# Optimization experiments

Hardware: AMD Instinct MI355X
Metric: run time of the kernel (lower is better)

## Reference

```python
import jax, jax.numpy as jnp
import numpy as np

B, I, J, C, H = 1, 384, 384, 128, 4
CH = 128          # overall hidden
HD = CH // H      # 32 per head
INF = 1000000000.0
EPS = 1e-5


def setup_inputs() -> dict:
    key = jax.random.key(0)
    ks = jax.random.split(key, 10)
    s = 0.02
    return {
        "x": jax.random.normal(ks[0], (B, I, J, C), dtype=jnp.float32),
        "mask": jnp.ones((B, I, J), dtype=jnp.float32),
        "ln_w": jnp.ones((C,), dtype=jnp.float32),
        "ln_b": jnp.zeros((C,), dtype=jnp.float32),
        "wz": jax.random.normal(ks[1], (C, H), dtype=jnp.float32) * s,
        "bz": jnp.zeros((H,), dtype=jnp.float32),
        "wq": jax.random.normal(ks[2], (C, CH), dtype=jnp.float32) * s,
        "wk": jax.random.normal(ks[3], (C, CH), dtype=jnp.float32) * s,
        "wv": jax.random.normal(ks[4], (C, CH), dtype=jnp.float32) * s,
        "wg": jax.random.normal(ks[5], (C, CH), dtype=jnp.float32) * s,
        "bg": jnp.ones((CH,), dtype=jnp.float32),
        "wo": jax.random.normal(ks[6], (CH, C), dtype=jnp.float32) * s,
        "bo": jnp.zeros((C,), dtype=jnp.float32),
    }


def _layer_norm(x, w, b):
    mu = jnp.mean(x, axis=-1, keepdims=True)
    var = jnp.mean(jnp.square(x - mu), axis=-1, keepdims=True)
    return (x - mu) * jax.lax.rsqrt(var + EPS) * w + b


def reference(x, mask, ln_w, ln_b, wz, bz, wq, wk, wv, wg, bg, wo, bo):
    # starting=True: attention over last row axis J
    x = _layer_norm(x, ln_w, ln_b)                      # [B,I,J,C]
    mask_bias = (INF * (mask - 1.0))[:, :, None, None, :]   # [B,I,1,1,J]
    # triangle bias: linear_z then permute (2,0,1), unsqueeze(-4) -> [B,1,H,I,J]
    tri_bias = jnp.einsum("bijc,ch->bhij", x, wz) + bz[None, :, None, None]
    tri_bias = tri_bias[:, None]                        # [B,1,H,I,J]

    q = jnp.einsum("bijc,cd->bijd", x, wq).reshape(B, I, J, H, HD)
    k = jnp.einsum("bijc,cd->bijd", x, wk).reshape(B, I, J, H, HD)
    v = jnp.einsum("bijc,cd->bijd", x, wv).reshape(B, I, J, H, HD)
    q = q / jnp.sqrt(jnp.float32(HD))

    a = jnp.einsum("biqhd,bikhd->bihqk", q, k)          # [B,I,H,J,J]
    a = a + mask_bias + tri_bias
    a = jax.nn.softmax(a, axis=-1)
    o = jnp.einsum("bihqk,bikhd->biqhd", a, v)          # [B,I,J,H,HD]

    g = jax.nn.sigmoid(jnp.einsum("bijc,cd->bijd", x, wg) + bg)
    o = o.reshape(B, I, J, CH) * g
    return jnp.einsum("bijd,dc->bijc", o, wo) + bo      # [B,I,J,C]
```

## Files before the change

kernel.cpp:

```cpp
#include <hip/hip_runtime.h>
#include <math.h>

#define I_DIM 384
#define C_DIM 128
#define H_NUM 4
#define HD_DIM 32
#define M_DIM (I_DIM*I_DIM)
#define INF_F 1000000000.0f
#define EPS_F 1e-5f
#define QSCALE 0.17677669529663687f

typedef __attribute__((ext_vector_type(8))) short short8;
typedef __attribute__((ext_vector_type(4))) float f32x4;
union U4S8 { uint4 u; short8 s; };

__device__ __forceinline__ unsigned short f2bf(float f) {
    unsigned int u = __float_as_uint(f);
    u += 0x7fffu + ((u >> 16) & 1u);
    return (unsigned short)(u >> 16);
}
__device__ __forceinline__ float bf2f(unsigned short h) {
    return __uint_as_float((unsigned int)h << 16);
}
__device__ __forceinline__ unsigned int pk2(float a, float b) {
    return (unsigned int)f2bf(a) | ((unsigned int)f2bf(b) << 16);
}
__device__ __forceinline__ unsigned int cvtpk(float lo, float hi) {
    unsigned int r;
    asm("v_cvt_pk_bf16_f32 %0, %1, %2" : "=v"(r) : "v"(lo), "v"(hi));
    return r;
}

__device__ uint4 wfmt_dev[5*4096];

__device__ __forceinline__ void load_lds16(const uint4* gp, void* lp) {
    __builtin_amdgcn_global_load_lds(
        (const __attribute__((address_space(1))) unsigned int*)gp,
        (__attribute__((address_space(3))) unsigned int*)lp,
        16, 0, 0);
}

__global__ __launch_bounds__(256) void wprep_kernel(
    const float* __restrict__ wq, const float* __restrict__ wk,
    const float* __restrict__ wg, const float* __restrict__ wv,
    const float* __restrict__ wo)
{
    const int tid  = blockIdx.x*256 + threadIdx.x;
    const int l    = tid & 63, tile = tid >> 6;
    const int ks   = tile & 3, nt = (tile >> 2) & 7;
    const int s    = (tile >> 5) & 1, m = tile >> 6;
    const float* W = (m==0)?wq:(m==1)?wk:(m==2)?wg:(m==3)?wv:wo;
    const float scale = (m==0) ? QSCALE : 1.f;
    const int n  = nt*16 + (l & 15);
    const int kb = ks*32 + (l >> 4)*8;
    unsigned int hw[4];
    #pragma unroll
    for (int jp = 0; jp < 4; ++jp) {
        unsigned short hs[2];
        #pragma unroll
        for (int e = 0; e < 2; ++e) {
            float v = W[(size_t)(kb + jp*2 + e)*C_DIM + n] * scale;
            unsigned short h = f2bf(v);
            if (s) h = f2bf(v - bf2f(h));
            hs[e] = h;
        }
        hw[jp] = (unsigned int)hs[0] | ((unsigned int)hs[1] << 16);
    }
    wfmt_dev[(size_t)m*4096 + (size_t)((s*8 + nt)*4 + ks)*64 + l] =
        make_uint4(hw[0], hw[1], hw[2], hw[3]);
}

__global__ __launch_bounds__(256, 4) void ln_proj_kernel(
    const float* __restrict__ x,
    const float* __restrict__ lnw, const float* __restrict__ lnb,
    const float* __restrict__ wz,  const float* __restrict__ bz,
    const float* __restrict__ bg,
    float* __restrict__ qo, unsigned short* __restrict__ ko16,
    unsigned int* __restrict__ vto, float* __restrict__ go,
    float* __restrict__ zo)
{
    __shared__ __align__(16) unsigned int xs[4096];
    __shared__ __align__(16) uint4 wbuf4[1024];
    unsigned int* vts = xs;

    const int t    = threadIdx.x;
    const int row0 = blockIdx.x * 64;
    const int w = t >> 6, l = t & 63, n16 = l & 15, quad = l >> 4;

    #pragma unroll
    for (int it = 0; it < 4; ++it) {
        const int tl = w*4 + it;
        const int s = tl >> 3, ntl = (tl >> 2) & 1, ks = tl & 3;
        load_lds16(wfmt_dev + (size_t)((s*8 + ntl)*4 + ks)*64 + l,
                   (char*)wbuf4 + tl*1024);
    }

    float4 xv[8];
    const int r = t >> 2, qt = t & 3, c0 = qt * 32;
    const int sw = (r & 7) << 2;
    {
        const float* xrow = x + (size_t)(row0 + r)*C_DIM + c0;
        float s = 0.f, ss = 0.f;
        #pragma unroll
        for (int i2 = 0; i2 < 8; i2++) {
            xv[i2] = ((const float4*)xrow)[i2];
            s  += xv[i2].x + xv[i2].y + xv[i2].z + xv[i2].w;
            ss += xv[i2].x*xv[i2].x + xv[i2].y*xv[i2].y
                + xv[i2].z*xv[i2].z + xv[i2].w*xv[i2].w;
        }
        s  += __shfl_xor(s, 1);  s  += __shfl_xor(s, 2);
        ss += __shfl_xor(ss, 1); ss += __shfl_xor(ss, 2);
        const float mean = s * (1.f/128.f);
        const float var  = ss * (1.f/128.f) - mean*mean;
        const float rstd = rsqrtf(var + EPS_F);
        const float4* wz4 = (const float4*)wz;
        float4 zacc = make_float4(0.f,0.f,0.f,0.f);
        #pragma unroll
        for (int i2 = 0; i2 < 8; i2++) {
            float4 w4 = ((const float4*)(lnw + c0))[i2];
            float4 b4 = ((const float4*)(lnb + c0))[i2];
            float4 r4;
            r4.x = (xv[i2].x - mean)*rstd*w4.x + b4.x;
            r4.y = (xv[i2].y - mean)*rstd*w4.y + b4.y;
            r4.z = (xv[i2].z - mean)*rstd*w4.z + b4.z;
            r4.w = (xv[i2].w - mean)*rstd*w4.w + b4.w;
            const float4 za = wz4[c0 + i2*4 + 0];
            const float4 zb_ = wz4[c0 + i2*4 + 1];
            const float4 zc = wz4[c0 + i2*4 + 2];
            const float4 zd = wz4[c0 + i2*4 + 3];
            zacc.x += r4.x*za.x + r4.y*zb_.x + r4.z*zc.x + r4.w*zd.x;
            zacc.y += r4.x*za.y + r4.y*zb_.y + r4.z*zc.y + r4.w*zd.y;
            zacc.z += r4.x*za.z + r4.y*zb_.z + r4.z*zc.z + r4.w*zd.z;
            zacc.w += r4.x*za.w + r4.y*zb_.w + r4.z*zc.w + r4.w*zd.w;
            const int wi = r*64 + qt*16 + i2*2;
            xs[(wi  ) ^ sw] = pk2(r4.x, r4.y);
            xs[(wi+1) ^ sw] = pk2(r4.z, r4.w);
            xv[i2] = r4;
        }
        zacc.x += __shfl_xor(zacc.x, 1); zacc.x += __shfl_xor(zacc.x, 2);
        zacc.y += __shfl_xor(zacc.y, 1); zacc.y += __shfl_xor(zacc.y, 2);
        zacc.z += __shfl_xor(zacc.z, 1); zacc.z += __shfl_xor(zacc.z, 2);
        zacc.w += __shfl_xor(zacc.w, 1); zacc.w += __shfl_xor(zacc.w, 2);
        const float zv = (qt==0)?zacc.x:(qt==1)?zacc.y:(qt==2)?zacc.z:zacc.w;
        zo[(size_t)qt*M_DIM + row0 + r] = zv + bz[qt];
    }
    __syncthreads();

    U4S8 ah[4], al[4];
    const int arow = w*16 + n16;
    #pragma unroll
    for (int ks = 0; ks < 4; ++ks) {
        const int bofs = arow*256 + ((ks*64 + quad*16) ^ ((arow & 7) << 4));
        ah[ks].u = *(const uint4*)((const char*)xs + bofs);
    }
    __syncthreads();

    #pragma unroll
    for (int i2 = 0; i2 < 8; i2++) {
        const float4 r4 = xv[i2];
        const unsigned short h0 = f2bf(r4.x), h1 = f2bf(r4.y),
                             h2 = f2bf(r4.z), h3 = f2bf(r4.w);
        const int wi = r*64 + qt*16 + i2*2;
        xs[(wi  ) ^ sw] = (unsigned int)f2bf(r4.x - bf2f(h0))
                        | ((unsigned int)f2bf(r4.y - bf2f(h1)) << 16);
        xs[(wi+1) ^ sw] = (unsigned int)f2bf(r4.z - bf2f(h2))
                        | ((unsigned int)f2bf(r4.w - bf2f(h3)) << 16);
    }
    __syncthreads();
    #pragma unroll
    for (int ks = 0; ks < 4; ++ks) {
        const int bofs = arow*256 + ((ks*64 + quad*16) ^ ((arow & 7) << 4));
        al[ks].u = *(const uint4*)((const char*)xs + bofs);
    }

    const int i_blk = row0 / I_DIM;
    const int jp0   = (row0 % I_DIM) >> 1;
    const int rw0   = row0 + w*16 + quad*4;

    #pragma unroll
    for (int rd = 0; rd < 16; ++rd) {
        const int mi = rd >> 2, qq = rd & 3;

        f32x4 acc[2];
        #pragma unroll
        for (int ntl = 0; ntl < 2; ++ntl) {
            f32x4 a = {0.f, 0.f, 0.f, 0.f};
            #pragma unroll
            for (int ks = 0; ks < 4; ++ks) {
                U4S8 bh, bl;
                bh.u = wbuf4[(    ntl*4 + ks)*64 + l];
                bl.u = wbuf4[(8 + ntl*4 + ks)*64 + l];
                a = __builtin_amdgcn_mfma_f32_16x16x32_bf16(ah[ks].s, bh.s, a, 0,0,0);
                a = __builtin_amdgcn_mfma_f32_16x16x32_bf16(al[ks].s, bh.s, a, 0,0,0);
                a = __builtin_amdgcn_mfma_f32_16x16x32_bf16(ah[ks].s, bl.s, a, 0,0,0);
            }
            acc[ntl] = a;
        }

        if (mi == 0) {
            #pragma unroll
            for (int ntl = 0; ntl < 2; ++ntl)
                #pragma unroll
                for (int rr = 0; rr < 4; ++rr)
                    qo[(size_t)(rw0 + rr)*C_DIM + qq*32 + ntl*16 + n16] =
                        acc[ntl][rr];
        } else if (mi == 1) {
            #pragma unroll
            for (int ntl = 0; ntl < 2; ++ntl)
                #pragma unroll
                for (int rr = 0; rr < 4; ++rr)
                    ko16[(size_t)(rw0 + rr)*C_DIM + qq*32 + ntl*16 + n16] =
                        f2bf(acc[ntl][rr]);
        } else if (mi == 2) {
            #pragma unroll
            for (int ntl = 0; ntl < 2; ++ntl) {
                const float bgv = bg[qq*32 + ntl*16 + n16];
                #pragma unroll
                for (int rr = 0; rr < 4; ++rr)
                    go[(size_t)(rw0 + rr)*C_DIM + qq*32 + ntl*16 + n16] =
                        1.f/(1.f + __expf(-(acc[ntl][rr] + bgv)));
            }
        } else {
            #pragma unroll
            for (int ntl = 0; ntl < 2; ++ntl)
                #pragma unroll
                for (int pr = 0; pr < 2; ++pr)
                    vts[(ntl*16 + n16)*33 + w*8 + quad*2 + pr] =
                        pk2(acc[ntl][2*pr], acc[ntl][2*pr+1]);
            __syncthreads();
            for (int idx = t; idx < 32*32; idx += 256) {
                const int ch_l = idx >> 5, p = idx & 31;
                vto[((size_t)i_blk*C_DIM + qq*32 + ch_l)*192 + jp0 + p] =
                    vts[ch_l*33 + p];
            }
        }

        __syncthreads();
        if (rd < 15) {
            const int m2 = (rd+1) >> 2, q2 = (rd+1) & 3;
            #pragma unroll
            for (int it = 0; it < 4; ++it) {
                const int tl = w*4 + it;
                const int s = tl >> 3, ntl2 = (tl >> 2) & 1, ks = tl & 3;
                load_lds16(wfmt_dev + (size_t)m2*4096
                           + (size_t)((s*8 + (q2*2 + ntl2))*4 + ks)*64 + l,
                           (char*)wbuf4 + tl*1024);
            }
        }
        __syncthreads();
    }
}

__global__ __launch_bounds__(256, 3) void attn_mfma_kernel(
    const float* q, const unsigned short* __restrict__ k16,
    const unsigned int* __restrict__ vt32, const float* __restrict__ zb,
    const float* __restrict__ mask, float* o)
{
    __shared__ uint4 Ks4[384*4];
    __shared__ uint4 VTl[32*49];
    __shared__ __align__(16) float mbl[384];

    const int ii = blockIdx.x;
    const int h  = blockIdx.y;
    const int t  = threadIdx.x;
    const size_t rbase = (size_t)ii*I_DIM*C_DIM + h*HD_DIM;

    for (int idx = t; idx < 1536; idx += 256) {
        const int j = idx >> 2, c4 = idx & 3;
        Ks4[j*4 + (c4 ^ ((j >> 1) & 3))] =
            ((const uint4*)k16)[rbase/8 + (size_t)j*16 + c4];
    }
    for (int idx = t; idx < 1536; idx += 256) {
        const int d = idx / 48, m = idx - d*48;
        VTl[d*49 + m] = ((const uint4*)vt32)[((size_t)ii*C_DIM + h*HD_DIM + d)*48 + m];
    }
    for (int jj = t; jj < 384; jj += 256)
        mbl[jj] = INF_F * (mask[(size_t)ii*I_DIM + jj] - 1.f);
    __syncthreads();

    const int w = t >> 6, l = t & 63;
    const int n16 = l & 15, quad = l >> 4;
    const int slA = n16 + ((quad & 1) << 5);
    const int slB = slA + 16;
    const bool hi = (quad & 2) != 0;

    #pragma unroll 1
    for (int qt = 0; qt < 6; qt++) {
        const int qg = w*6 + qt;

        U4S8 a;
        {
            const float* qrow = q + rbase + (size_t)(qg*16 + n16)*C_DIM + quad*8;
            const float4 f0 = ((const float4*)qrow)[0];
            const float4 f1 = ((const float4*)qrow)[1];
            a.u = make_uint4(cvtpk(f0.x,f0.y), cvtpk(f0.z,f0.w),
                             cvtpk(f1.x,f1.y), cvtpk(f1.z,f1.w));
        }

        f32x4 oacc0 = {0.f,0.f,0.f,0.f}, oacc1 = {0.f,0.f,0.f,0.f};
        float lsum = 0.f;
        const float* zrow = zb + (size_t)h*M_DIM
                          + (size_t)(qg*16 + n16)*I_DIM + quad*4;

        #pragma unroll 1
        for (int c = 0; c < 4; c++) {
            float4 zc4[6];
            #pragma unroll
            for (int k6 = 0; k6 < 6; k6++)
                zc4[k6] = *(const float4*)&zrow[96*c + k6*16];
            float4 mb4[6];
            #pragma unroll
            for (int k6 = 0; k6 < 6; k6++)
                mb4[k6] = *(const float4*)&mbl[96*c + k6*16 + quad*4];

            f32x4 accS[6];
            #pragma unroll
            for (int k6 = 0; k6 < 6; k6++) {
                const int key = (6*c + k6)*16 + n16;
                U4S8 b;
                b.u = Ks4[key*4 + (quad ^ ((key >> 1) & 3))];
                accS[k6] = __builtin_amdgcn_mfma_f32_16x16x32_bf16(
                    b.s, a.s, (f32x4){0.f,0.f,0.f,0.f}, 0, 0, 0);
            }

            unsigned int pu[6][2];
            #pragma unroll
            for (int k6 = 0; k6 < 6; k6++) {
                const float e0 = __expf(accS[k6][0] + zc4[k6].x + mb4[k6].x);
                const float e1 = __expf(accS[k6][1] + zc4[k6].y + mb4[k6].y);
                const float e2 = __expf(accS[k6][2] + zc4[k6].z + mb4[k6].z);
                const float e3 = __expf(accS[k6][3] + zc4[k6].w + mb4[k6].w);
                lsum += (e0 + e1) + (e2 + e3);
                pu[k6][0] = cvtpk(e0, e1);
                pu[k6][1] = cvtpk(e2, e3);
            }

            #pragma unroll
            for (int km = 0; km < 3; km++) {
                const unsigned int x0 = __shfl((int)pu[2*km  ][0], slA);
                const unsigned int x1 = __shfl((int)pu[2*km+1][0], slA);
                const unsigned int y0 = __shfl((int)pu[2*km  ][1], slA);
                const unsigned int y1 = __shfl((int)pu[2*km+1][1], slA);
                const unsigned int z0 = __shfl((int)pu[2*km  ][0], slB);
                const unsigned int z1 = __shfl((int)pu[2*km+1][0], slB);
                const unsigned int w0 = __shfl((int)pu[2*km  ][1], slB);
                const unsigned int w1 = __shfl((int)pu[2*km+1][1], slB);
                U4S8 pa;
                pa.u = make_uint4(hi?x1:x0, hi?y1:y0, hi?z1:z0, hi?w1:w0);
                U4S8 vb0, vb1;
                vb0.u = VTl[(n16     )*49 + quad + 4*km + 12*c];
                vb1.u = VTl[(16 + n16)*49 + quad + 4*km + 12*c];
                oacc0 = __builtin_amdgcn_mfma_f32_16x16x32_bf16(vb0.s, pa.s, oacc0, 0,0,0);
                oacc1 = __builtin_amdgcn_mfma_f32_16x16x32_bf16(vb1.s, pa.s, oacc1, 0,0,0);
            }
        }

        float s_ = lsum;
        s_ += __shfl_xor(s_, 16);
        s_ += __shfl_xor(s_, 32);
        const float rcp = 1.f / s_;
        const size_t orow = rbase + (size_t)(qg*16 + n16)*C_DIM;
        float4 o0 = make_float4(oacc0[0]*rcp, oacc0[1]*rcp,
                                oacc0[2]*rcp, oacc0[3]*rcp);
        float4 o1 = make_float4(oacc1[0]*rcp, oacc1[1]*rcp,
                                oacc1[2]*rcp, oacc1[3]*rcp);
        *(float4*)&o[orow + quad*4]      = o0;
        *(float4*)&o[orow + 16 + quad*4] = o1;
    }
}

__global__ __launch_bounds__(256, 4) void out_proj_kernel(
    const float* __restrict__ o, const float* g,
    const float* __restrict__ bo, float* out)
{
    __shared__ __align__(16) unsigned int xs[4096];
    __shared__ __align__(16) uint4 wbuf4[1024];
    const int t    = threadIdx.x;
    const int row0 = blockIdx.x * 64;
    const int w = t >> 6, l = t & 63, n16 = l & 15, quad = l >> 4;

    #pragma unroll
    for (int it = 0; it < 4; ++it) {
        const int tl = w*4 + it;
        const int s = tl >> 3, ntl = (tl >> 2) & 1, ks = tl & 3;
        load_lds16(wfmt_dev + (size_t)4*4096 + (size_t)((s*8 + ntl)*4 + ks)*64 + l,
                   (char*)wbuf4 + tl*1024);
    }

    float4 pv[8];
    const int r = t >> 2, qt = t & 3, c0 = qt * 32;
    const int sw = (r & 7) << 2;
    {
        const float4* orow = (const float4*)(o + (size_t)(row0 + r)*C_DIM + c0);
        const float4* grow = (const float4*)(g + (size_t)(row0 + r)*C_DIM + c0);
        #pragma unroll
        for (int i2 = 0; i2 < 8; i2++) {
            const float4 a = orow[i2];
            const float4 b = grow[i2];
            float4 p;
            p.x = a.x*b.x; p.y = a.y*b.y; p.z = a.z*b.z; p.w = a.w*b.w;
            const int wi = r*64 + qt*16 + i2*2;
            xs[(wi  ) ^ sw] = pk2(p.x, p.y);
            xs[(wi+1) ^ sw] = pk2(p.z, p.w);
            pv[i2] = p;
        }
    }
    __syncthreads();

    U4S8 ah[4], al[4];
    const int arow = w*16 + n16;
    #pragma unroll
    for (int ks = 0; ks < 4; ++ks) {
        const int bofs = arow*256 + ((ks*64 + quad*16) ^ ((arow & 7) << 4));
        ah[ks].u = *(const uint4*)((const char*)xs + bofs);
    }
    __syncthreads();
    #pragma unroll
    for (int i2 = 0; i2 < 8; i2++) {
        const float4 p = pv[i2];
        const unsigned short h0 = f2bf(p.x), h1 = f2bf(p.y),
                             h2 = f2bf(p.z), h3 = f2bf(p.w);
        const int wi = r*64 + qt*16 + i2*2;
        xs[(wi  ) ^ sw] = (unsigned int)f2bf(p.x - bf2f(h0))
                        | ((unsigned int)f2bf(p.y - bf2f(h1)) << 16);
        xs[(wi+1) ^ sw] = (unsigned int)f2bf(p.z - bf2f(h2))
                        | ((unsigned int)f2bf(p.w - bf2f(h3)) << 16);
    }
    __syncthreads();
    #pragma unroll
    for (int ks = 0; ks < 4; ++ks) {
        const int bofs = arow*256 + ((ks*64 + quad*16) ^ ((arow & 7) << 4));
        al[ks].u = *(const uint4*)((const char*)xs + bofs);
    }

    const int rw0 = row0 + w*16 + quad*4;
    #pragma unroll
    for (int qq = 0; qq < 4; ++qq) {
        f32x4 acc[2];
        #pragma unroll
        for (int ntl = 0; ntl < 2; ++ntl) {
            f32x4 a = {0.f, 0.f, 0.f, 0.f};
            #pragma unroll
            for (int ks = 0; ks < 4; ++ks) {
                U4S8 bh, bl;
                bh.u = wbuf4[(    ntl*4 + ks)*64 + l];
                bl.u = wbuf4[(8 + ntl*4 + ks)*64 + l];
                a = __builtin_amdgcn_mfma_f32_16x16x32_bf16(ah[ks].s, bh.s, a, 0,0,0);
                a = __builtin_amdgcn_mfma_f32_16x16x32_bf16(al[ks].s, bh.s, a, 0,0,0);
                a = __builtin_amdgcn_mfma_f32_16x16x32_bf16(ah[ks].s, bl.s, a, 0,0,0);
            }
            acc[ntl] = a;
        }
        #pragma unroll
        for (int ntl = 0; ntl < 2; ++ntl) {
            const int n = qq*32 + ntl*16 + n16;
            const float bov = bo[n];
            #pragma unroll
            for (int rr = 0; rr < 4; ++rr)
                out[(size_t)(rw0 + rr)*C_DIM + n] = acc[ntl][rr] + bov;
        }
        __syncthreads();
        if (qq < 3) {
            const int q2 = qq + 1;
            #pragma unroll
            for (int it = 0; it < 4; ++it) {
                const int tl = w*4 + it;
                const int s = tl >> 3, ntl2 = (tl >> 2) & 1, ks = tl & 3;
                load_lds16(wfmt_dev + (size_t)4*4096
                           + (size_t)((s*8 + (q2*2 + ntl2))*4 + ks)*64 + l,
                           (char*)wbuf4 + tl*1024);
            }
        }
        __syncthreads();
    }
}

extern "C" void kernel_launch(void* const* d_in, const int* in_sizes, int n_in,
                              void* d_out, int out_size, void* d_ws, size_t ws_size,
                              hipStream_t stream)
{
    (void)in_sizes; (void)n_in; (void)out_size; (void)ws_size;
    const float* x    = (const float*)d_in[0];
    const float* mask = (const float*)d_in[1];
    const float* lnw  = (const float*)d_in[2];
    const float* lnb  = (const float*)d_in[3];
    const float* wz   = (const float*)d_in[4];
    const float* bz   = (const float*)d_in[5];
    const float* wq   = (const float*)d_in[6];
    const float* wk   = (const float*)d_in[7];
    const float* wv   = (const float*)d_in[8];
    const float* wg   = (const float*)d_in[9];
    const float* bg   = (const float*)d_in[10];
    const float* wo   = (const float*)d_in[11];
    const float* bo   = (const float*)d_in[12];

    float* ws = (float*)d_ws;
    float* qb   = ws;
    float* zbuf = qb + (size_t)M_DIM*C_DIM;
    unsigned short* kb16 = (unsigned short*)(zbuf + (size_t)H_NUM*M_DIM);
    unsigned int*   vt32 = (unsigned int*)(kb16 + (size_t)M_DIM*C_DIM);
    float* gbuf = (float*)d_out;

    wprep_kernel<<<80, 256, 0, stream>>>(wq, wk, wg, wv, wo);
    ln_proj_kernel<<<M_DIM/64, 256, 0, stream>>>(
        x, lnw, lnb, wz, bz, bg, qb, kb16, vt32, gbuf, zbuf);
    attn_mfma_kernel<<<dim3(I_DIM, H_NUM), 256, 0, stream>>>(
        qb, kb16, vt32, zbuf, mask, qb );
    out_proj_kernel<<<M_DIM/64, 256, 0, stream>>>(
        qb, gbuf, bo, (float*)d_out);
}
```

Baseline: 440.9 us.

## Double-buffer weight tiles, use exp2 softmax, read K from global, swizzle V LDS

The projection and output kernels now double-buffer the weight tiles in LDS. The next tile's async load is issued before the current MFMA work, and one barrier per iteration is dropped. This doubles weight LDS and lowers launch-bounds occupancy from 4 to 3. The attention kernel folds log2(e) into the Q scale, triangle bias and mask so it can use the native exp2. It reads K fragments straight from global instead of staging them in LDS, and stores V^T in a swizzled fragment layout to avoid bank conflicts, with occupancy raised to 4.

```diff
diff --git a/kernel.cpp b/kernel.cpp
--- a/kernel.cpp
+++ b/kernel.cpp
@@ -9,6 +9,7 @@
 #define INF_F 1000000000.0f
 #define EPS_F 1e-5f
 #define QSCALE 0.17677669529663687f
+#define LOG2E_F 1.4426950408889634f
 
 typedef __attribute__((ext_vector_type(8))) short short8;
 typedef __attribute__((ext_vector_type(4))) float f32x4;
@@ -50,7 +51,7 @@
     const int ks   = tile & 3, nt = (tile >> 2) & 7;
     const int s    = (tile >> 5) & 1, m = tile >> 6;
     const float* W = (m==0)?wq:(m==1)?wk:(m==2)?wg:(m==3)?wv:wo;
-    const float scale = (m==0) ? QSCALE : 1.f;
+    const float scale = (m==0) ? QSCALE*LOG2E_F : 1.f;
     const int n  = nt*16 + (l & 15);
     const int kb = ks*32 + (l >> 4)*8;
     unsigned int hw[4];
@@ -70,7 +71,7 @@
         make_uint4(hw[0], hw[1], hw[2], hw[3]);
 }
 
-__global__ __launch_bounds__(256, 4) void ln_proj_kernel(
+__global__ __launch_bounds__(256, 3) void ln_proj_kernel(
     const float* __restrict__ x,
     const float* __restrict__ lnw, const float* __restrict__ lnb,
     const float* __restrict__ wz,  const float* __restrict__ bz,
@@ -80,7 +81,7 @@
     float* __restrict__ zo)
 {
     __shared__ __align__(16) unsigned int xs[4096];
-    __shared__ __align__(16) uint4 wbuf4[1024];
+    __shared__ __align__(16) uint4 wbuf4[2048];
     unsigned int* vts = xs;
 
     const int t    = threadIdx.x;
@@ -142,7 +143,7 @@
         zacc.z += __shfl_xor(zacc.z, 1); zacc.z += __shfl_xor(zacc.z, 2);
         zacc.w += __shfl_xor(zacc.w, 1); zacc.w += __shfl_xor(zacc.w, 2);
         const float zv = (qt==0)?zacc.x:(qt==1)?zacc.y:(qt==2)?zacc.z:zacc.w;
-        zo[(size_t)qt*M_DIM + row0 + r] = zv + bz[qt];
+        zo[(size_t)qt*M_DIM + row0 + r] = (zv + bz[qt]) * LOG2E_F;
     }
     __syncthreads();
 
@@ -177,10 +178,23 @@
     const int jp0   = (row0 % I_DIM) >> 1;
     const int rw0   = row0 + w*16 + quad*4;
 
+    int p = 0;
     #pragma unroll
     for (int rd = 0; rd < 16; ++rd) {
         const int mi = rd >> 2, qq = rd & 3;
 
+        if (rd < 15) {
+            const int m2 = (rd+1) >> 2, q2 = (rd+1) & 3;
+            #pragma unroll
+            for (int it = 0; it < 4; ++it) {
+                const int tl = w*4 + it;
+                const int s = tl >> 3, ntl2 = (tl >> 2) & 1, ks = tl & 3;
+                load_lds16(wfmt_dev + (size_t)m2*4096
+                           + (size_t)((s*8 + (q2*2 + ntl2))*4 + ks)*64 + l,
+                           (char*)wbuf4 + (p^1)*16384 + tl*1024);
+            }
+        }
+
         f32x4 acc[2];
         #pragma unroll
         for (int ntl = 0; ntl < 2; ++ntl) {
@@ -188,8 +202,8 @@
             #pragma unroll
             for (int ks = 0; ks < 4; ++ks) {
                 U4S8 bh, bl;
-                bh.u = wbuf4[(    ntl*4 + ks)*64 + l];
-                bl.u = wbuf4[(8 + ntl*4 + ks)*64 + l];
+                bh.u = wbuf4[p*1024 + (    ntl*4 + ks)*64 + l];
+                bl.u = wbuf4[p*1024 + (8 + ntl*4 + ks)*64 + l];
                 a = __builtin_amdgcn_mfma_f32_16x16x32_bf16(ah[ks].s, bh.s, a, 0,0,0);
                 a = __builtin_amdgcn_mfma_f32_16x16x32_bf16(al[ks].s, bh.s, a, 0,0,0);
                 a = __builtin_amdgcn_mfma_f32_16x16x32_bf16(ah[ks].s, bl.s, a, 0,0,0);
@@ -229,35 +243,23 @@
                         pk2(acc[ntl][2*pr], acc[ntl][2*pr+1]);
             __syncthreads();
             for (int idx = t; idx < 32*32; idx += 256) {
-                const int ch_l = idx >> 5, p = idx & 31;
-                vto[((size_t)i_blk*C_DIM + qq*32 + ch_l)*192 + jp0 + p] =
-                    vts[ch_l*33 + p];
+                const int ch_l = idx >> 5, pp = idx & 31;
+                vto[((size_t)i_blk*C_DIM + qq*32 + ch_l)*192 + jp0 + pp] =
+                    vts[ch_l*33 + pp];
             }
         }
 
         __syncthreads();
-        if (rd < 15) {
-            const int m2 = (rd+1) >> 2, q2 = (rd+1) & 3;
-            #pragma unroll
-            for (int it = 0; it < 4; ++it) {
-                const int tl = w*4 + it;
-                const int s = tl >> 3, ntl2 = (tl >> 2) & 1, ks = tl & 3;
-                load_lds16(wfmt_dev + (size_t)m2*4096
-                           + (size_t)((s*8 + (q2*2 + ntl2))*4 + ks)*64 + l,
-                           (char*)wbuf4 + tl*1024);
-            }
-        }
-        __syncthreads();
-    }
-}
-
-__global__ __launch_bounds__(256, 3) void attn_mfma_kernel(
+        p ^= 1;
+    }
+}
+
+__global__ __launch_bounds__(256, 4) void attn_mfma_kernel(
     const float* q, const unsigned short* __restrict__ k16,
     const unsigned int* __restrict__ vt32, const float* __restrict__ zb,
     const float* __restrict__ mask, float* o)
 {
-    __shared__ uint4 Ks4[384*4];
-    __shared__ uint4 VTl[32*49];
+    __shared__ uint4 VTf[24*64];
     __shared__ __align__(16) float mbl[384];
 
     const int ii = blockIdx.x;
@@ -266,16 +268,18 @@
     const size_t rbase = (size_t)ii*I_DIM*C_DIM + h*HD_DIM;
 
     for (int idx = t; idx < 1536; idx += 256) {
-        const int j = idx >> 2, c4 = idx & 3;
-        Ks4[j*4 + (c4 ^ ((j >> 1) & 3))] =
-            ((const uint4*)k16)[rbase/8 + (size_t)j*16 + c4];
-    }
-    for (int idx = t; idx < 1536; idx += 256) {
         const int d = idx / 48, m = idx - d*48;
-        VTl[d*49 + m] = ((const uint4*)vt32)[((size_t)ii*C_DIM + h*HD_DIM + d)*48 + m];
+        const int c = m / 12, rr = m - c*12;
+        const int km = rr >> 2, qd = rr & 3;
+        const int hh = d >> 4, nn = d & 15;
+        const int f  = (c*3 + km)*2 + hh;
+        const int l0 = qd*16 + nn;
+        const int lp = l0 ^ ((l0 >> 3) & 7) ^ ((3*c + km) & 7);
+        VTf[f*64 + lp] =
+            ((const uint4*)vt32)[((size_t)ii*C_DIM + h*HD_DIM + d)*48 + m];
     }
     for (int jj = t; jj < 384; jj += 256)
-        mbl[jj] = INF_F * (mask[(size_t)ii*I_DIM + jj] - 1.f);
+        mbl[jj] = (INF_F*LOG2E_F) * (mask[(size_t)ii*I_DIM + jj] - 1.f);
     __syncthreads();
 
     const int w = t >> 6, l = t & 63;
@@ -283,6 +287,8 @@
     const int slA = n16 + ((quad & 1) << 5);
     const int slB = slA + 16;
     const bool hi = (quad & 2) != 0;
+    const int lswz = l ^ ((l >> 3) & 7);
+    const unsigned short* kf = k16 + rbase + (size_t)n16*C_DIM + quad*8;
 
     #pragma unroll 1
     for (int qt = 0; qt < 6; qt++) {
@@ -304,6 +310,10 @@
 
         #pragma unroll 1
         for (int c = 0; c < 4; c++) {
+            U4S8 kb[6];
+            #pragma unroll
+            for (int k6 = 0; k6 < 6; k6++)
+                kb[k6].u = *(const uint4*)(kf + (size_t)((6*c + k6)*16)*C_DIM);
             float4 zc4[6];
             #pragma unroll
             for (int k6 = 0; k6 < 6; k6++)
@@ -315,21 +325,17 @@
 
             f32x4 accS[6];
             #pragma unroll
+            for (int k6 = 0; k6 < 6; k6++)
+                accS[k6] = __builtin_amdgcn_mfma_f32_16x16x32_bf16(
+                    kb[k6].s, a.s, (f32x4){0.f,0.f,0.f,0.f}, 0, 0, 0);
+
+            unsigned int pu[6][2];
+            #pragma unroll
             for (int k6 = 0; k6 < 6; k6++) {
-                const int key = (6*c + k6)*16 + n16;
-                U4S8 b;
-                b.u = Ks4[key*4 + (quad ^ ((key >> 1) & 3))];
-                accS[k6] = __builtin_amdgcn_mfma_f32_16x16x32_bf16(
-                    b.s, a.s, (f32x4){0.f,0.f,0.f,0.f}, 0, 0, 0);
-            }
-
-            unsigned int pu[6][2];
-            #pragma unroll
-            for (int k6 = 0; k6 < 6; k6++) {
-                const float e0 = __expf(accS[k6][0] + zc4[k6].x + mb4[k6].x);
-                const float e1 = __expf(accS[k6][1] + zc4[k6].y + mb4[k6].y);
-                const float e2 = __expf(accS[k6][2] + zc4[k6].z + mb4[k6].z);
-                const float e3 = __expf(accS[k6][3] + zc4[k6].w + mb4[k6].w);
+                const float e0 = __builtin_amdgcn_exp2f(accS[k6][0] + zc4[k6].x + mb4[k6].x);
+                const float e1 = __builtin_amdgcn_exp2f(accS[k6][1] + zc4[k6].y + mb4[k6].y);
+                const float e2 = __builtin_amdgcn_exp2f(accS[k6][2] + zc4[k6].z + mb4[k6].z);
+                const float e3 = __builtin_amdgcn_exp2f(accS[k6][3] + zc4[k6].w + mb4[k6].w);
                 lsum += (e0 + e1) + (e2 + e3);
                 pu[k6][0] = cvtpk(e0, e1);
                 pu[k6][1] = cvtpk(e2, e3);
@@ -347,9 +353,10 @@
                 const unsigned int w1 = __shfl((int)pu[2*km+1][1], slB);
                 U4S8 pa;
                 pa.u = make_uint4(hi?x1:x0, hi?y1:y0, hi?z1:z0, hi?w1:w0);
+                const int mix = (3*c + km) & 7;
                 U4S8 vb0, vb1;
-                vb0.u = VTl[(n16     )*49 + quad + 4*km + 12*c];
-                vb1.u = VTl[(16 + n16)*49 + quad + 4*km + 12*c];
+                vb0.u = VTf[((c*3 + km)*2    )*64 + (lswz ^ mix)];
+                vb1.u = VTf[((c*3 + km)*2 + 1)*64 + (lswz ^ mix)];
                 oacc0 = __builtin_amdgcn_mfma_f32_16x16x32_bf16(vb0.s, pa.s, oacc0, 0,0,0);
                 oacc1 = __builtin_amdgcn_mfma_f32_16x16x32_bf16(vb1.s, pa.s, oacc1, 0,0,0);
             }
@@ -369,12 +376,12 @@
     }
 }
 
-__global__ __launch_bounds__(256, 4) void out_proj_kernel(
+__global__ __launch_bounds__(256, 3) void out_proj_kernel(
     const float* __restrict__ o, const float* g,
     const float* __restrict__ bo, float* out)
 {
     __shared__ __align__(16) unsigned int xs[4096];
-    __shared__ __align__(16) uint4 wbuf4[1024];
+    __shared__ __align__(16) uint4 wbuf4[2048];
     const int t    = threadIdx.x;
     const int row0 = blockIdx.x * 64;
     const int w = t >> 6, l = t & 63, n16 = l & 15, quad = l >> 4;
@@ -434,32 +441,9 @@
     }
 
     const int rw0 = row0 + w*16 + quad*4;
+    int p = 0;
     #pragma unroll
     for (int qq = 0; qq < 4; ++qq) {
-        f32x4 acc[2];
-        #pragma unroll
-        for (int ntl = 0; ntl < 2; ++ntl) {
-            f32x4 a = {0.f, 0.f, 0.f, 0.f};
-            #pragma unroll
-            for (int ks = 0; ks < 4; ++ks) {
-                U4S8 bh, bl;
-                bh.u = wbuf4[(    ntl*4 + ks)*64 + l];
-                bl.u = wbuf4[(8 + ntl*4 + ks)*64 + l];
-                a = __builtin_amdgcn_mfma_f32_16x16x32_bf16(ah[ks].s, bh.s, a, 0,0,0);
-                a = __builtin_amdgcn_mfma_f32_16x16x32_bf16(al[ks].s, bh.s, a, 0,0,0);
-                a = __builtin_amdgcn_mfma_f32_16x16x32_bf16(ah[ks].s, bl.s, a, 0,0,0);
-            }
-            acc[ntl] = a;
-        }
-        #pragma unroll
-        for (int ntl = 0; ntl < 2; ++ntl) {
-            const int n = qq*32 + ntl*16 + n16;
-            const float bov = bo[n];
-            #pragma unroll
-            for (int rr = 0; rr < 4; ++rr)
-                out[(size_t)(rw0 + rr)*C_DIM + n] = acc[ntl][rr] + bov;
-        }
-        __syncthreads();
         if (qq < 3) {
             const int q2 = qq + 1;
             #pragma unroll
@@ -468,10 +452,34 @@
                 const int s = tl >> 3, ntl2 = (tl >> 2) & 1, ks = tl & 3;
                 load_lds16(wfmt_dev + (size_t)4*4096
                            + (size_t)((s*8 + (q2*2 + ntl2))*4 + ks)*64 + l,
-                           (char*)wbuf4 + tl*1024);
-            }
+                           (char*)wbuf4 + (p^1)*16384 + tl*1024);
+            }
+        }
+        f32x4 acc[2];
+        #pragma unroll
+        for (int ntl = 0; ntl < 2; ++ntl) {
+            f32x4 a = {0.f, 0.f, 0.f, 0.f};
+            #pragma unroll
+            for (int ks = 0; ks < 4; ++ks) {
+                U4S8 bh, bl;
+                bh.u = wbuf4[p*1024 + (    ntl*4 + ks)*64 + l];
+                bl.u = wbuf4[p*1024 + (8 + ntl*4 + ks)*64 + l];
+                a = __builtin_amdgcn_mfma_f32_16x16x32_bf16(ah[ks].s, bh.s, a, 0,0,0);
+                a = __builtin_amdgcn_mfma_f32_16x16x32_bf16(al[ks].s, bh.s, a, 0,0,0);
+                a = __builtin_amdgcn_mfma_f32_16x16x32_bf16(ah[ks].s, bl.s, a, 0,0,0);
+            }
+            acc[ntl] = a;
+        }
+        #pragma unroll
+        for (int ntl = 0; ntl < 2; ++ntl) {
+            const int n = qq*32 + ntl*16 + n16;
+            const float bov = bo[n];
+            #pragma unroll
+            for (int rr = 0; rr < 4; ++rr)
+                out[(size_t)(rw0 + rr)*C_DIM + n] = acc[ntl][rr] + bov;
         }
         __syncthreads();
+        p ^= 1;
     }
 }
 
```

New measurement: 511.6 us. 1.16x slower.
